# Performance work log

Measured on AMD Instinct MI355X. Metric: run time of the kernel, lower is better.

Reference implementation:

```python
import jax, jax.numpy as jnp
import numpy as np

TAU = 0.01          # gumbel_softmax temperature
EPS = 1e-7          # tf.keras.backend.epsilon()
DEPTH = 5
N_NODES = 2 ** DEPTH - 1   # 31 internal nodes
N_LEAVES = 2 ** DEPTH      # 32 leaves


def _build_route():
    # route[l, node + dir*N_NODES] = 1 along the root-to-leaf path of leaf l
    # (same structure old_route_to_new_route produces for a perfect tree)
    route = np.zeros((N_LEAVES, 2 * N_NODES), dtype=np.float32)
    for l in range(N_LEAVES):
        node = 0
        for d in range(DEPTH):
            bit = (l >> (DEPTH - 1 - d)) & 1  # 0 = left, 1 = right
            route[l, node + bit * N_NODES] = 1.0
            node = 2 * node + 1 + bit
    return route


def setup_inputs() -> dict:
    B, F, T = 32768, 128, 100
    key = jax.random.key(0)
    k1, k2, k3, k4 = jax.random.split(key, 4)
    x = jax.random.normal(k1, (B, F), dtype=jnp.float32)
    kernel = jax.random.normal(k2, (T, F, N_NODES), dtype=jnp.float32) * 0.1
    bias = jax.random.normal(k3, (T, N_NODES), dtype=jnp.float32) * 0.1
    leaf = jax.random.normal(k4, (T, N_LEAVES), dtype=jnp.float32)
    route = jnp.asarray(_build_route())  # [L, 2N], shared tree topology
    return {"x": x, "kernel": kernel, "bias": bias, "leaf": leaf, "route": route}


def reference(x, kernel, bias, leaf, route):
    # NodeLayer: matmul(x, concat([K, -K], 1)) + concat([b, -b], 0)
    h = jnp.einsum("bf,tfn->btn", x, kernel) + bias          # [B, T, N]
    h2 = jnp.concatenate([h, -h], axis=-1)                   # [B, T, 2N]
    # activation1: log(clip(sigmoid(clip(h/tau, -32, 32)), eps, 1))
    a1 = jnp.log(jnp.clip(jax.nn.sigmoid(jnp.clip(h2 / TAU, -32.0, 32.0)), EPS, 1.0))
    # route aggregation: sum log-probs along each root->leaf path
    r = jnp.einsum("btm,lm->btl", a1, route)                 # [B, T, L]
    # activation2: exp(clip(., -32, 0)) -> leaf routing probabilities
    probs = jnp.exp(jnp.clip(r, -32.0, 0.0))
    # weight leaf values by route probabilities, sum over leaves and trees
    return jnp.einsum("btl,tl->b", probs, leaf)              # [B] raw GBM output
```

## Files before the change

### kernel.cpp

```cpp
#include <hip/hip_runtime.h>

typedef _Float16 f16x8 __attribute__((ext_vector_type(8)));
typedef float    f32x4 __attribute__((ext_vector_type(4)));

#define NTREES  100
#define WAVES   8
#define NCH     13
#define BM      64
#define SCALE   144.269504088896f

#define H_OFF  16384
#define LDS_BYTES 49152

__device__ __forceinline__ float exp2_fast(float v) {
#if __has_builtin(__builtin_amdgcn_exp2f)
  return __builtin_amdgcn_exp2f(v);
#else
  return exp2f(v);
#endif
}

__device__ __forceinline__ void sig2(float z, float& sl, float& sr) {
  z = fmaxf(z, -24.0f);
  float e = exp2_fast(-z);
  sl = __builtin_amdgcn_rcpf(1.0f + e);
  sr = e * sl;
}

__global__ void prep_b(const float* __restrict__ kern, const float* __restrict__ bias,
                       unsigned short* __restrict__ bws, float* __restrict__ bias_s) {
  __shared__ float kt[128][33];
  const int t = blockIdx.x, tid = threadIdx.x;
  const float* src = kern + (size_t)t * (128 * 31);
  for (int i = tid; i < 128 * 31; i += 256) {
    int f = i / 31, n = i - f * 31;
    kt[f][n] = src[i] * SCALE;
  }
  for (int f = tid; f < 128; f += 256) kt[f][31] = 0.0f;
  if (tid < 32)
    bias_s[t * 32 + tid] = (tid < 31) ? bias[t * 31 + tid] * SCALE : 0.0f;
  __syncthreads();
  unsigned short* dst = bws + (size_t)t * 4096;
  for (int s = tid; s < 512; s += 256) {
    const int ks = s >> 7, frag = (s >> 6) & 1, lane = s & 63;
    const int n  = (frag << 4) + (lane & 15);
    const int k0 = ks * 32 + ((lane >> 4) << 3);
    f16x8 o;
    #pragma unroll
    for (int j = 0; j < 8; ++j) o[j] = (_Float16)kt[k0 + j][n];
    *(f16x8*)(dst + s * 8) = o;
  }
}

__global__ __launch_bounds__(512, 4) void gbm_main(
    const float* __restrict__ x,
    const unsigned short* __restrict__ bws,
    const float* __restrict__ bias_s,
    const float* __restrict__ leaf,
    float* __restrict__ out)
{
  __shared__ __align__(16) unsigned char lds[LDS_BYTES];
  float* red = (float*)lds;

  const int tid  = threadIdx.x;
  const int lane = tid & 63;
  const int w    = tid >> 6;
  const int rowbase = blockIdx.x * BM;

  {
    const int row = (w << 3) + (lane >> 3);
    #pragma unroll
    for (int kh = 0; kh < 2; ++kh) {
      const int k = kh * 64 + ((lane & 7) << 3);
      const float* px = x + (size_t)(rowbase + row) * 128 + k;
      float4 v0 = *(const float4*)(px);
      float4 v1 = *(const float4*)(px + 4);
      float vals[8] = {v0.x, v0.y, v0.z, v0.w, v1.x, v1.y, v1.z, v1.w};
      f16x8 h8;
      #pragma unroll
      for (int j = 0; j < 8; ++j) h8[j] = (_Float16)vals[j];
      const int off = ((((row >> 4) << 2) + (k >> 5)) * 64 +
                       (row & 15) + (((k >> 3) & 3) << 4)) * 16;
      *(f16x8*)(lds + off) = h8;
    }
  }

  const int abase = lane * 16;
  const int hr = (lane >> 4) << 2;
  const int hc = lane & 15;
  int wb[4];
  #pragma unroll
  for (int r = 0; r < 4; ++r)
    wb[r] = H_OFF + (w << 12) +
            ((((hr + r) << 6) + (hc << 2)) ^ ((((hr >> 1) + (r >> 1)) & 7) << 4));
  const int rbase0 = H_OFF + (w << 12) + ((lane << 6) ^ (((lane >> 1) & 7) << 4));

  const unsigned short* bbase = bws + (size_t)w * 4096;
  f16x8 breg[8];
  #pragma unroll
  for (int i = 0; i < 8; ++i)
    breg[i] = *(const f16x8*)(bbase + (size_t)i * 512 + lane * 8);

  __syncthreads();

  float outAcc = 0.0f;

  for (int c = 0; c < NCH; ++c) {
    const int tree = c * WAVES + w;
    const bool act = (tree < NTREES);

    f32x4 acc[4][2] = {};
    float bv0 = 0.0f, bv1 = 0.0f;
    if (act) {
      bv0 = bias_s[tree * 32 + hc];
      bv1 = bias_s[tree * 32 + 16 + hc];

      __builtin_amdgcn_s_setprio(1);
      #pragma unroll
      for (int ks = 0; ks < 4; ++ks) {
        f16x8 b0 = breg[ks * 2], b1 = breg[ks * 2 + 1];
        #pragma unroll
        for (int rt = 0; rt < 4; ++rt) {
          f16x8 ah = *(const f16x8*)(lds + abase + (rt * 4 + ks) * 1024);
          acc[rt][0] = __builtin_amdgcn_mfma_f32_16x16x32_f16(ah, b0, acc[rt][0], 0, 0, 0);
          acc[rt][1] = __builtin_amdgcn_mfma_f32_16x16x32_f16(ah, b1, acc[rt][1], 0, 0, 0);
        }
      }
      __builtin_amdgcn_s_setprio(0);
    }

    if ((c + 1) * WAVES + w < NTREES) {
      const unsigned short* nb = bbase + (size_t)(c + 1) * (WAVES * 4096);
      #pragma unroll
      for (int i = 0; i < 8; ++i)
        breg[i] = *(const f16x8*)(nb + (size_t)i * 512 + lane * 8);
    }

    if (act) {
      #pragma unroll
      for (int rt = 0; rt < 4; ++rt)
        #pragma unroll
        for (int r = 0; r < 4; ++r) {
          unsigned z0 = __float_as_uint(acc[rt][0][r] + bv0);
          unsigned z1 = __float_as_uint(acc[rt][1][r] + bv1);
          *(unsigned*)(lds + wb[r] + rt * 1024) = __builtin_amdgcn_perm(z1, z0, 0x07060302u);
        }

      unsigned hvu[16];
      #pragma unroll
      for (int g = 0; g < 4; ++g) {
        uint4 q = *(const uint4*)(lds + (rbase0 ^ (g << 4)));
        hvu[g * 4 + 0] = q.x; hvu[g * 4 + 1] = q.y;
        hvu[g * 4 + 2] = q.z; hvu[g * 4 + 3] = q.w;
      }
#define ZV(n) __uint_as_float(((n) < 16) ? (hvu[(n)] << 16) : (hvu[(n) - 16] & 0xffff0000u))

      const float* lp = leaf + (size_t)__builtin_amdgcn_readfirstlane(tree) * 32;
      float cum[16];
      cum[0] = 1.0f;
      #pragma unroll
      for (int d = 0; d < 4; ++d) {
        #pragma unroll
        for (int i = (1 << d) - 1; i >= 0; --i) {
          const int node = (1 << d) - 1 + i;
          float sl, sr;
          sig2(ZV(node), sl, sr);
          float cl = cum[i];
          cum[2 * i]     = cl * sl;
          cum[2 * i + 1] = cl * sr;
        }
      }
      float s = 0.0f;
      #pragma unroll
      for (int i = 0; i < 16; ++i) {
        const int node = 15 + i;
        float sl, sr;
        sig2(ZV(node), sl, sr);
        s = fmaf(cum[i], fmaf(sl, lp[2 * i], sr * lp[2 * i + 1]), s);
      }
      outAcc += s;
#undef ZV
    }
  }

  __syncthreads();
  red[tid] = outAcc;
  __syncthreads();
  if (tid < 64) {
    float s = red[tid];
    #pragma unroll
    for (int sidx = 1; sidx < WAVES; ++sidx)
      s += red[sidx * 64 + tid];
    out[rowbase + tid] = s;
  }
}

extern "C" void kernel_launch(void* const* d_in, const int* in_sizes, int n_in,
                              void* d_out, int out_size, void* d_ws, size_t ws_size,
                              hipStream_t stream) {
  const float* x    = (const float*)d_in[0];
  const float* kern = (const float*)d_in[1];
  const float* bias = (const float*)d_in[2];
  const float* leaf = (const float*)d_in[3];

  unsigned short* bws = (unsigned short*)d_ws;
  float* bias_s = (float*)((unsigned char*)d_ws + 819200);

  prep_b<<<NTREES, 256, 0, stream>>>(kern, bias, bws, bias_s);
  gbm_main<<<32768 / BM, 512, 0, stream>>>(x, bws, bias_s, leaf, (float*)d_out);
}
```

Measured before the change: 59.08 us.

## Split each tree across two lanes per row with permuted node layout and smaller row tile

Halves the row tile to 32 rows per block so each wave's 64 lanes cover 32 rows × two half-trees. Each lane walks one root-to-depth-2 subtree path and its own half of the leaves. The prep kernel permutes and sign-flips the node columns so each half-lane's nodes are contiguous, and stores fp32 instead of packed bf16-ish halves. The aim is less serial sigmoid work per lane and higher occupancy (launch bounds 6). The cost is redundant upper-level node evaluation, loss of the B-register prefetch across chunks, and twice as many blocks reloading weights.

```diff
diff --git a/kernel.cpp b/kernel.cpp
--- a/kernel.cpp
+++ b/kernel.cpp
@@ -2,15 +2,16 @@
 
 typedef _Float16 f16x8 __attribute__((ext_vector_type(8)));
 typedef float    f32x4 __attribute__((ext_vector_type(4)));
+typedef float    f32x2 __attribute__((ext_vector_type(2)));
 
 #define NTREES  100
 #define WAVES   8
 #define NCH     13
-#define BM      64
+#define BM      32
 #define SCALE   144.269504088896f
 
-#define H_OFF  16384
-#define LDS_BYTES 49152
+#define H_OFF   8192
+#define LDS_BYTES (H_OFF + WAVES * 4096)
 
 __device__ __forceinline__ float exp2_fast(float v) {
 #if __has_builtin(__builtin_amdgcn_exp2f)
@@ -27,23 +28,35 @@
   sr = e * sl;
 }
 
+__device__ __forceinline__ int node_perm(int sc, float& sg) {
+  const int half = sc >> 4, c = sc & 15;
+  sg = 1.0f;
+  if (c == 0) { if (half) sg = -1.0f; return 0; }
+  if (c == 1) return 1 + half;
+  if (c < 4)  return 1 + 2 * half + c;
+  if (c < 8)  return 3 + 4 * half + c;
+  return 7 + 8 * half + c;
+}
+
 __global__ void prep_b(const float* __restrict__ kern, const float* __restrict__ bias,
                        unsigned short* __restrict__ bws, float* __restrict__ bias_s) {
   __shared__ float kt[128][33];
   const int t = blockIdx.x, tid = threadIdx.x;
   const float* src = kern + (size_t)t * (128 * 31);
-  for (int i = tid; i < 128 * 31; i += 256) {
-    int f = i / 31, n = i - f * 31;
-    kt[f][n] = src[i] * SCALE;
-  }
-  for (int f = tid; f < 128; f += 256) kt[f][31] = 0.0f;
-  if (tid < 32)
-    bias_s[t * 32 + tid] = (tid < 31) ? bias[t * 31 + tid] * SCALE : 0.0f;
+  for (int i = tid; i < 128 * 32; i += 256) {
+    const int f = i >> 5, sc = i & 31;
+    float sg; const int g = node_perm(sc, sg);
+    kt[f][sc] = src[f * 31 + g] * (SCALE * sg);
+  }
+  if (tid < 32) {
+    float sg; const int g = node_perm(tid, sg);
+    bias_s[t * 32 + tid] = bias[t * 31 + g] * (SCALE * sg);
+  }
   __syncthreads();
   unsigned short* dst = bws + (size_t)t * 4096;
   for (int s = tid; s < 512; s += 256) {
-    const int ks = s >> 7, frag = (s >> 6) & 1, lane = s & 63;
-    const int n  = (frag << 4) + (lane & 15);
+    const int ks = s >> 7, fr = (s >> 6) & 1, lane = s & 63;
+    const int n  = (fr << 4) + (lane & 15);
     const int k0 = ks * 32 + ((lane >> 4) << 3);
     f16x8 o;
     #pragma unroll
@@ -52,7 +65,7 @@
   }
 }
 
-__global__ __launch_bounds__(512, 4) void gbm_main(
+__global__ __launch_bounds__(512, 6) void gbm_main(
     const float* __restrict__ x,
     const unsigned short* __restrict__ bws,
     const float* __restrict__ bias_s,
@@ -68,38 +81,35 @@
   const int rowbase = blockIdx.x * BM;
 
   {
-    const int row = (w << 3) + (lane >> 3);
-    #pragma unroll
-    for (int kh = 0; kh < 2; ++kh) {
-      const int k = kh * 64 + ((lane & 7) << 3);
-      const float* px = x + (size_t)(rowbase + row) * 128 + k;
-      float4 v0 = *(const float4*)(px);
-      float4 v1 = *(const float4*)(px + 4);
-      float vals[8] = {v0.x, v0.y, v0.z, v0.w, v1.x, v1.y, v1.z, v1.w};
-      f16x8 h8;
-      #pragma unroll
-      for (int j = 0; j < 8; ++j) h8[j] = (_Float16)vals[j];
-      const int off = ((((row >> 4) << 2) + (k >> 5)) * 64 +
-                       (row & 15) + (((k >> 3) & 3) << 4)) * 16;
-      *(f16x8*)(lds + off) = h8;
-    }
+    const int row = tid >> 4;
+    const int k   = (tid & 15) << 3;
+    const float* px = x + (size_t)(rowbase + row) * 128 + k;
+    float4 v0 = *(const float4*)px;
+    float4 v1 = *(const float4*)(px + 4);
+    float vals[8] = {v0.x, v0.y, v0.z, v0.w, v1.x, v1.y, v1.z, v1.w};
+    f16x8 h8;
+    #pragma unroll
+    for (int j = 0; j < 8; ++j) h8[j] = (_Float16)vals[j];
+    const int frag = ((row >> 4) << 2) + (k >> 5);
+    const int lnn  = (row & 15) + (((k >> 3) & 3) << 4);
+    *(f16x8*)(lds + (frag * 64 + lnn) * 16) = h8;
   }
 
   const int abase = lane * 16;
-  const int hr = (lane >> 4) << 2;
-  const int hc = lane & 15;
-  int wb[4];
+  const int hc = lane & 15, hr = (lane >> 4) << 2;
+  int wb[4][2];
   #pragma unroll
   for (int r = 0; r < 4; ++r)
-    wb[r] = H_OFF + (w << 12) +
-            ((((hr + r) << 6) + (hc << 2)) ^ ((((hr >> 1) + (r >> 1)) & 7) << 4));
-  const int rbase0 = H_OFF + (w << 12) + ((lane << 6) ^ (((lane >> 1) & 7) << 4));
-
-  const unsigned short* bbase = bws + (size_t)w * 4096;
-  f16x8 breg[8];
+    #pragma unroll
+    for (int ct = 0; ct < 2; ++ct)
+      wb[r][ct] = H_OFF + (w << 12) + ((hr + r) << 7) +
+                  (((ct << 6) + (hc << 2)) ^ (((hr + r) & 7) << 4));
+  const int rrow = lane & 31, rhalf = lane >> 5;
+  int rb[4];
   #pragma unroll
-  for (int i = 0; i < 8; ++i)
-    breg[i] = *(const f16x8*)(bbase + (size_t)i * 512 + lane * 8);
+  for (int g = 0; g < 4; ++g)
+    rb[g] = H_OFF + (w << 12) + (rrow << 7) +
+            (((rhalf << 6) + (g << 4)) ^ ((rrow & 7) << 4));
 
   __syncthreads();
 
@@ -107,90 +117,88 @@
 
   for (int c = 0; c < NCH; ++c) {
     const int tree = c * WAVES + w;
-    const bool act = (tree < NTREES);
-
-    f32x4 acc[4][2] = {};
-    float bv0 = 0.0f, bv1 = 0.0f;
+    const bool act = tree < NTREES;
+    const int tt = act ? tree : (NTREES - 1);
+
+    f16x8 breg[8];
+    const unsigned short* bt = bws + (size_t)tt * 4096;
+    #pragma unroll
+    for (int i = 0; i < 8; ++i)
+      breg[i] = *(const f16x8*)(bt + (size_t)i * 512 + lane * 8);
+
+    const float bv0 = bias_s[tt * 32 + hc];
+    const float bv1 = bias_s[tt * 32 + 16 + hc];
+
     if (act) {
-      bv0 = bias_s[tree * 32 + hc];
-      bv1 = bias_s[tree * 32 + 16 + hc];
-
+      f32x4 acc[2][2] = {};
       __builtin_amdgcn_s_setprio(1);
       #pragma unroll
       for (int ks = 0; ks < 4; ++ks) {
         f16x8 b0 = breg[ks * 2], b1 = breg[ks * 2 + 1];
         #pragma unroll
-        for (int rt = 0; rt < 4; ++rt) {
+        for (int rt = 0; rt < 2; ++rt) {
           f16x8 ah = *(const f16x8*)(lds + abase + (rt * 4 + ks) * 1024);
           acc[rt][0] = __builtin_amdgcn_mfma_f32_16x16x32_f16(ah, b0, acc[rt][0], 0, 0, 0);
           acc[rt][1] = __builtin_amdgcn_mfma_f32_16x16x32_f16(ah, b1, acc[rt][1], 0, 0, 0);
         }
       }
       __builtin_amdgcn_s_setprio(0);
-    }
-
-    if ((c + 1) * WAVES + w < NTREES) {
-      const unsigned short* nb = bbase + (size_t)(c + 1) * (WAVES * 4096);
-      #pragma unroll
-      for (int i = 0; i < 8; ++i)
-        breg[i] = *(const f16x8*)(nb + (size_t)i * 512 + lane * 8);
-    }
-
-    if (act) {
-      #pragma unroll
-      for (int rt = 0; rt < 4; ++rt)
+
+      #pragma unroll
+      for (int rt = 0; rt < 2; ++rt)
         #pragma unroll
-        for (int r = 0; r < 4; ++r) {
-          unsigned z0 = __float_as_uint(acc[rt][0][r] + bv0);
-          unsigned z1 = __float_as_uint(acc[rt][1][r] + bv1);
-          *(unsigned*)(lds + wb[r] + rt * 1024) = __builtin_amdgcn_perm(z1, z0, 0x07060302u);
-        }
-
-      unsigned hvu[16];
-      #pragma unroll
-      for (int g = 0; g < 4; ++g) {
-        uint4 q = *(const uint4*)(lds + (rbase0 ^ (g << 4)));
-        hvu[g * 4 + 0] = q.x; hvu[g * 4 + 1] = q.y;
-        hvu[g * 4 + 2] = q.z; hvu[g * 4 + 3] = q.w;
+        for (int ct = 0; ct < 2; ++ct)
+          #pragma unroll
+          for (int r = 0; r < 4; ++r)
+            *(float*)(lds + wb[r][ct] + rt * 2048) = acc[rt][ct][r] + (ct ? bv1 : bv0);
+
+      f32x4 h0 = *(const f32x4*)(lds + rb[0]);
+      f32x4 h1 = *(const f32x4*)(lds + rb[1]);
+
+      float sl, sr;
+      sig2(h0[0], sl, sr);
+      const float c0 = sl;
+      sig2(h0[1], sl, sr);
+      const float a0 = c0 * sl, a1 = c0 * sr;
+      sig2(h0[2], sl, sr);
+      const float b0_ = a0 * sl, b1_ = a0 * sr;
+      sig2(h0[3], sl, sr);
+      const float b2_ = a1 * sl, b3_ = a1 * sr;
+      float cum[8];
+      sig2(h1[0], sl, sr); cum[0] = b0_ * sl; cum[1] = b0_ * sr;
+      sig2(h1[1], sl, sr); cum[2] = b1_ * sl; cum[3] = b1_ * sr;
+      sig2(h1[2], sl, sr); cum[4] = b2_ * sl; cum[5] = b2_ * sr;
+      sig2(h1[3], sl, sr); cum[6] = b3_ * sl; cum[7] = b3_ * sr;
+
+      f32x4 h2 = *(const f32x4*)(lds + rb[2]);
+      f32x4 h3 = *(const f32x4*)(lds + rb[3]);
+      const f32x2* lp2 = (const f32x2*)(leaf + (size_t)tree * 32 + (rhalf << 4));
+
+      float s = 0.0f;
+      #pragma unroll
+      for (int i = 0; i < 4; ++i) {
+        sig2(h2[i], sl, sr);
+        f32x2 lv = lp2[i];
+        s = fmaf(cum[i], fmaf(sl, lv[0], sr * lv[1]), s);
       }
-#define ZV(n) __uint_as_float(((n) < 16) ? (hvu[(n)] << 16) : (hvu[(n) - 16] & 0xffff0000u))
-
-      const float* lp = leaf + (size_t)__builtin_amdgcn_readfirstlane(tree) * 32;
-      float cum[16];
-      cum[0] = 1.0f;
-      #pragma unroll
-      for (int d = 0; d < 4; ++d) {
-        #pragma unroll
-        for (int i = (1 << d) - 1; i >= 0; --i) {
-          const int node = (1 << d) - 1 + i;
-          float sl, sr;
-          sig2(ZV(node), sl, sr);
-          float cl = cum[i];
-          cum[2 * i]     = cl * sl;
-          cum[2 * i + 1] = cl * sr;
-        }
-      }
-      float s = 0.0f;
-      #pragma unroll
-      for (int i = 0; i < 16; ++i) {
-        const int node = 15 + i;
-        float sl, sr;
-        sig2(ZV(node), sl, sr);
-        s = fmaf(cum[i], fmaf(sl, lp[2 * i], sr * lp[2 * i + 1]), s);
+      #pragma unroll
+      for (int i = 0; i < 4; ++i) {
+        sig2(h3[i], sl, sr);
+        f32x2 lv = lp2[4 + i];
+        s = fmaf(cum[4 + i], fmaf(sl, lv[0], sr * lv[1]), s);
       }
       outAcc += s;
-#undef ZV
     }
   }
 
   __syncthreads();
   red[tid] = outAcc;
   __syncthreads();
-  if (tid < 64) {
-    float s = red[tid];
-    #pragma unroll
-    for (int sidx = 1; sidx < WAVES; ++sidx)
-      s += red[sidx * 64 + tid];
+  if (tid < 32) {
+    float s = 0.0f;
+    #pragma unroll
+    for (int j = 0; j < 16; ++j)
+      s += red[j * 32 + tid];
     out[rowbase + tid] = s;
   }
 }
```

After: 62.26 us. 5.4% more time.
